# Optimization experiments

Hardware: AMD Instinct MI355X
Metric: run time of the kernel (lower is better)

Reference implementation:

```python
import jax, jax.numpy as jnp
import numpy as np

N = 100000   # nodes
E = 1600000  # edges
D = 128      # input_dim
H = 128      # hidden_dim
CH = 16      # cluster_hidden_dim
P = 10       # processor_nodes


def setup_inputs() -> dict:
    key = jax.random.key(0)
    ks = jax.random.split(key, 22)
    s = 0.05
    return {
        "x": jax.random.normal(ks[0], (N, D), jnp.float32),
        "edges": jax.random.randint(ks[1], (2, E), 0, N, dtype=jnp.int32),
        "edge_attr": jax.random.uniform(ks[2], (E,), jnp.float32),
        "ready": jax.random.randint(ks[3], (N, 1), 0, 2, dtype=jnp.int32),
        "proc_emb": jax.random.normal(ks[4], (P, 3), jnp.float32),
        # GCN layers (PyG GCNConv: lin without bias, explicit bias added after aggregation)
        "gcn_w": jax.random.normal(ks[5], (2, D, H), jnp.float32) * s,
        "gcn_b": jax.random.normal(ks[6], (2, H), jnp.float32) * s,
        # listmlp: Linear(H,H) -> relu, then Linear(H,1)
        "mlp_w1": jax.random.normal(ks[7], (H, H), jnp.float32) * s,
        "mlp_b1": jax.random.normal(ks[8], (H,), jnp.float32) * s,
        "mlp_w2": jax.random.normal(ks[9], (H, 1), jnp.float32) * s,
        "mlp_b2": jax.random.normal(ks[10], (1,), jnp.float32) * s,
        # listmlp_value: Linear(H,1)
        "val_w": jax.random.normal(ks[11], (H, 1), jnp.float32) * s,
        "val_b": jax.random.normal(ks[12], (1,), jnp.float32) * s,
        # cluster_linear: Linear(3*P, CH)
        "cl_w": jax.random.normal(ks[13], (3 * P, CH), jnp.float32) * s,
        "cl_b": jax.random.normal(ks[14], (CH,), jnp.float32) * s,
        # listmlp_pass: Linear(H+CH,H) -> relu, then Linear(H,1)
        "pass_w1": jax.random.normal(ks[15], (H + CH, H), jnp.float32) * s,
        "pass_b1": jax.random.normal(ks[16], (H,), jnp.float32) * s,
        "pass_w2": jax.random.normal(ks[17], (H, 1), jnp.float32) * s,
        "pass_b2": jax.random.normal(ks[18], (1,), jnp.float32) * s,
    }


def _gcn_layer(x, row, col, w_e, W, b):
    # PyG GCNConv with flow='target_to_source': out[row] += norm_e * (x @ W)[col]
    # gcn_norm with idx=row: deg[i] = sum of edge weights with row==i (self-loops included)
    h = x @ W                                              # [N,H]
    deg = jax.ops.segment_sum(w_e, row, num_segments=N)    # [N]
    dis = jnp.where(deg > 0, jax.lax.rsqrt(deg), 0.0)      # deg^-1/2, inf -> 0
    norm = dis[row] * w_e * dis[col]                       # [E+N]
    msg = h[col] * norm[:, None]                           # [E+N,H] gather
    out = jax.ops.segment_sum(msg, row, num_segments=N)    # [N,H] scatter-add
    return out + b


def _forward(x, edges, edge_attr, ready, proc_emb, gcn_w, gcn_b,
             mlp_w1, mlp_b1, mlp_w2, mlp_b2, val_w, val_b, cl_w, cl_b,
             pass_w1, pass_b1, pass_w2, pass_b2):
    # add self-loops with weight 1 (GCNConv default add_self_loops=True)
    loop = jnp.arange(N, dtype=edges.dtype)
    row = jnp.concatenate([edges[0], loop])
    col = jnp.concatenate([edges[1], loop])
    w_e = jnp.concatenate([edge_attr, jnp.ones((N,), edge_attr.dtype)])

    h = x
    for l in range(2):
        h = jax.nn.relu(_gcn_layer(h, row, col, w_e, gcn_w[l], gcn_b[l]))

    mask = ready[:, 0] > 0                                 # [N] bool
    v = jnp.mean(h, axis=0)                                # [H]
    x_pass = jnp.max(jnp.where(mask[:, None], h, -jnp.inf), axis=0)  # masked max, [H]

    fc = proc_emb.reshape(-1) @ cl_w + cl_b                # [CH]
    x_pass = jnp.concatenate([x_pass, fc], axis=0)         # [H+CH]

    v = v @ val_w + val_b                                  # [1]

    logits = jax.nn.relu(h @ mlp_w1 + mlp_b1) @ mlp_w2 + mlp_b2        # [N,1]
    x_pass = jax.nn.relu(x_pass @ pass_w1 + pass_b1) @ pass_w2 + pass_b2  # [1]

    # torch indexes logits[ready]; here we mask non-ready entries with -inf so
    # the softmax over [N+1] matches torch's values on the ready rows.
    node_logits = jnp.where(mask, logits[:, 0], -jnp.inf)
    probs = jax.nn.softmax(jnp.concatenate([node_logits, x_pass], axis=0))  # [N+1]
    return probs, v


def reference(x, edges, edge_attr, ready, proc_emb, gcn_w, gcn_b,
              mlp_w1, mlp_b1, mlp_w2, mlp_b2, val_w, val_b, cl_w, cl_b,
              pass_w1, pass_b1, pass_w2, pass_b2):
    return _forward(x, edges, edge_attr, ready, proc_emb, gcn_w, gcn_b,
                    mlp_w1, mlp_b1, mlp_w2, mlp_b2, val_w, val_b, cl_w, cl_b,
                    pass_w1, pass_b1, pass_w2, pass_b2)
```

## Files before the change

kernel.cpp:

```cpp
#include <hip/hip_runtime.h>
#include <cstdint>

#define NN 100000
#define EE 1600000
#define HH 128
#define NREP 8
#define PSZ (NN / 8)
#define HPP (PSZ / 2)
#define SS 64
#define CAP 300000
#define NBB 500
#define BCH 3200
#define SCAN_CHUNK 512
#define NSCAN ((NN + SCAN_CHUNK - 1) / SCAN_CHUNK)

typedef unsigned long long u64;
typedef unsigned short ushort;
typedef unsigned char uchar;
typedef __attribute__((ext_vector_type(8))) short bf16x8;
typedef __attribute__((ext_vector_type(4))) float f32x4;
typedef __attribute__((ext_vector_type(2))) float f32x2;

__device__ __forceinline__ void gl2lds16(const void* g, void* l) {
#if __has_builtin(__builtin_amdgcn_global_load_lds)
    __builtin_amdgcn_global_load_lds(
        (const __attribute__((address_space(1))) unsigned int*)g,
        (__attribute__((address_space(3))) unsigned int*)l, 16, 0, 0);
#else
    *(uint4*)l = *(const uint4*)g;
#endif
}

__device__ __forceinline__ ushort f2bf(float x) {
    union { float f; unsigned u; } v; v.f = x;
    unsigned r = v.u + 0x7fffu + ((v.u >> 16) & 1u);
    return (ushort)(r >> 16);
}
__device__ __forceinline__ float bf2f(unsigned h16) {
    union { unsigned u; float f; } v; v.u = h16 << 16; return v.f;
}

__device__ __forceinline__ uchar f2fp8(float a) {
    return (uchar)(__builtin_amdgcn_cvt_pk_fp8_f32(a, a, 0, false) & 0xff);
}
__device__ __forceinline__ void unpack8_fp8(uint2 q, float* v) {
    f32x2 a = __builtin_amdgcn_cvt_pk_f32_fp8(q.x, false);
    f32x2 b = __builtin_amdgcn_cvt_pk_f32_fp8(q.x, true);
    f32x2 c = __builtin_amdgcn_cvt_pk_f32_fp8(q.y, false);
    f32x2 d = __builtin_amdgcn_cvt_pk_f32_fp8(q.y, true);
    v[0] = a[0]; v[1] = a[1]; v[2] = b[0]; v[3] = b[1];
    v[4] = c[0]; v[5] = c[1]; v[6] = d[0]; v[7] = d[1];
}

__device__ __forceinline__ unsigned encf(float f) {
    int b = __float_as_int(f);
    return (b >= 0) ? ((unsigned)b | 0x80000000u) : ~(unsigned)b;
}
__device__ __forceinline__ float decf(unsigned u) {
    return (u & 0x80000000u) ? __int_as_float((int)(u & 0x7fffffffu))
                             : __int_as_float((int)(~u));
}
#define ENC_NEG_INF 0x007FFFFFu

__global__ void k_setup(float* __restrict__ meansum, unsigned* __restrict__ maxenc,
                        unsigned* __restrict__ lmaxenc, float* __restrict__ esum,
                        int* __restrict__ gtail,
                        const float* __restrict__ w0, const float* __restrict__ w1,
                        const float* __restrict__ w2, ushort* __restrict__ wt) {
    int idx = blockIdx.x * blockDim.x + threadIdx.x;
    if (idx < NREP * HH) { meansum[idx] = 0.f; maxenc[idx] = ENC_NEG_INF; }
    if (idx < 8) gtail[idx] = 0;
    if (idx == 0) { lmaxenc[0] = ENC_NEG_INF; esum[0] = 0.f; }
    if (idx < 3 * HH * HH) {
        int mat = idx >> 14;
        int e = idx & 16383;
        int n = e >> 7, k = e & 127;
        int g = k >> 3, el = k & 7;
        const float* src = (mat == 0) ? w0 : (mat == 1) ? w1 : w2;
        int pos = (mat << 14) | (n << 7) | (((g ^ (n & 15)) << 3) | el);
        wt[pos] = f2bf(src[k * HH + n]);
    }
}

__global__ __launch_bounds__(256) void k_bucket(const int* __restrict__ rows,
                                                const int* __restrict__ cols,
                                                const float* __restrict__ ea,
                                                int* __restrict__ gtail,
                                                u64* __restrict__ ebuck) {
    __shared__ u64 buf[8][1024];
    __shared__ int cnt8[8];
    __shared__ int rsv[8];
    int t = threadIdx.x;
    if (t < 8) cnt8[t] = 0;
    __syncthreads();
    int e0 = blockIdx.x * BCH;
    int e1 = e0 + BCH;
    for (int ebase = e0; ebase < e1; ebase += 1024) {
        int e = ebase + t * 4;
        if (e < e1) {
            int4 r4 = *(const int4*)(rows + e);
            int4 c4 = *(const int4*)(cols + e);
            float4 a4 = *(const float4*)(ea + e);
            int rr[4] = {r4.x, r4.y, r4.z, r4.w};
            int cc[4] = {c4.x, c4.y, c4.z, c4.w};
            float aa[4] = {a4.x, a4.y, a4.z, a4.w};
#pragma unroll
            for (int j = 0; j < 4; ++j) {
                int p = rr[j] / PSZ;
                int rl = rr[j] - p * PSZ;
                unsigned q = (unsigned)(aa[j] * 32767.0f + 0.5f);
                u64 en = ((u64)rl << 32) | (u64)(((unsigned)cc[j] << 15) | q);
                int idx = atomicAdd(&cnt8[p], 1);
                buf[p][idx] = en;
            }
        }
        __syncthreads();
        if (t < 8) rsv[t] = atomicAdd(&gtail[t], cnt8[t]);
        __syncthreads();
#pragma unroll
        for (int p = 0; p < 8; ++p) {
            int nn = cnt8[p], oo = rsv[p];
            u64* dst = ebuck + (size_t)p * CAP + oo;
            for (int j = t; j < nn; j += 256) dst[j] = buf[p][j];
        }
        __syncthreads();
        if (t < 8) cnt8[t] = 0;
        __syncthreads();
    }
}

__global__ __launch_bounds__(256) void k_cnt2(const u64* __restrict__ ebuck,
                                              const int* __restrict__ gtail,
                                              unsigned* __restrict__ cntp) {
    __shared__ unsigned h32[HPP];
    int b = blockIdx.x;
    int s = b >> 3, p = b & 7;
    for (int j = threadIdx.x; j < HPP; j += 256) h32[j] = 0;
    __syncthreads();
    int pc = gtail[p];
    int len = (pc + SS - 1) / SS;
    int lo = s * len, hi = min(lo + len, pc);
    const u64* src = ebuck + (size_t)p * CAP;
    for (int i = lo + threadIdx.x; i < hi; i += 256) {
        int rl = (int)(src[i] >> 32);
        atomicAdd(&h32[rl >> 1], (rl & 1) ? 0x10000u : 1u);
    }
    __syncthreads();
    unsigned* dst = cntp + (size_t)(p * SS + s) * HPP;
    for (int j = threadIdx.x; j < HPP; j += 256) dst[j] = h32[j];
}

__global__ void k_cntscan(const unsigned* __restrict__ cntp, int* __restrict__ count,
                          unsigned* __restrict__ deltap, int* __restrict__ basep,
                          int* __restrict__ bsum) {
    int b = blockIdx.x, t = threadIdx.x;
    int rp = b * 256 + t;
    int c0 = 0, c1 = 0;
    if (rp < NN / 2) {
        int p = rp / HPP, j = rp - p * HPP;
        unsigned s0 = 0, s1 = 0;
#pragma unroll 8
        for (int c = 0; c < SS; ++c) {
            size_t o = (size_t)(p * SS + c) * HPP + j;
            unsigned v = cntp[o];
            deltap[o] = s0 | (s1 << 16);
            s0 += v & 0xffffu;
            s1 += v >> 16;
        }
        c0 = (int)s0; c1 = (int)s1;
        *(int2*)(count + 2 * rp) = make_int2(c0, c1);
    }
    c0 = (c0 + 7) & ~7;
    c1 = (c1 + 7) & ~7;
    int s = c0 + c1;
    int lane = t & 63, w = t >> 6;
    int v = s;
#pragma unroll
    for (int off = 1; off < 64; off <<= 1) {
        int u = __shfl_up(v, off, 64);
        if (lane >= off) v += u;
    }
    __shared__ int wsum[4];
    if (lane == 63) wsum[w] = v;
    __syncthreads();
    int wadd = 0;
    for (int j = 0; j < w; ++j) wadd += wsum[j];
    int incl = v + wadd;
    int excl = incl - s;
    int i0 = 2 * rp;
    if (i0 < NN) basep[i0] = excl;
    if (i0 + 1 < NN) basep[i0 + 1] = excl + c0;
    if (t == 255) bsum[b] = incl;
}

__global__ void k_scan2(int* __restrict__ bsum, int* __restrict__ base) {
    __shared__ int tmp[256];
    int t = threadIdx.x;
    int v = (t < NSCAN) ? bsum[t] : 0;
    tmp[t] = v;
    __syncthreads();
    for (int off = 1; off < 256; off <<= 1) {
        int u = (t >= off) ? tmp[t - off] : 0;
        __syncthreads();
        tmp[t] += u;
        __syncthreads();
    }
    if (t == NSCAN - 1) base[NN] = tmp[t];
    if (t < NSCAN) bsum[t] = tmp[t] - v;
}

__global__ __launch_bounds__(256) void k_fill2(const u64* __restrict__ ebuck,
                                               const int* __restrict__ gtail,
                                               const unsigned* __restrict__ deltap,
                                               const int* __restrict__ basep,
                                               const int* __restrict__ bsum,
                                               unsigned* __restrict__ csre) {
    __shared__ int nxt[PSZ];
    int b = blockIdx.x;
    int s = b >> 3, p = b & 7;
    const unsigned* dsrc = deltap + (size_t)(p * SS + s) * HPP;
    const int* bsrc = basep + p * PSZ;
    for (int j = threadIdx.x; j < HPP; j += 256) {
        unsigned d = dsrc[j];
        int2 bb = *(const int2*)(bsrc + 2 * j);
        int badd = bsum[(p * PSZ + 2 * j) >> 9];
        nxt[2 * j] = bb.x + badd + (int)(d & 0xffffu);
        nxt[2 * j + 1] = bb.y + badd + (int)(d >> 16);
    }
    __syncthreads();
    int pc = gtail[p];
    int len = (pc + SS - 1) / SS;
    int lo = s * len, hi = min(lo + len, pc);
    const u64* src = ebuck + (size_t)p * CAP;
    for (int i = lo + threadIdx.x; i < hi; i += 256) {
        u64 en = src[i];
        int rl = (int)(en >> 32);
        int slot = atomicAdd(&nxt[rl], 1);
        csre[slot] = (unsigned)(en & 0xffffffffu);
    }
}

__global__ void k_degsum(const int* __restrict__ count, unsigned* __restrict__ csre,
                         const int* __restrict__ basep, const int* __restrict__ bsum,
                         int* __restrict__ base, float* __restrict__ dis) {
    int r = blockIdx.x * blockDim.x + threadIdx.x;
    if (r >= NN) return;
    int lo = basep[r] + bsum[r >> 9];
    int hip = (r == NN - 1) ? base[NN] : (basep[r + 1] + bsum[(r + 1) >> 9]);
    base[r] = lo;
    int hireal = lo + count[r];
    float s = 0.f;
    for (int e = lo; e < hireal; ++e) s += (float)(csre[e] & 0x7fffu);
    unsigned selfv = (unsigned)r << 15;
    for (int e = hireal; e < hip; ++e) csre[e] = selfv;
    dis[r] = rsqrtf(1.0f + s * (1.0f / 32767.0f));
}

__global__ __launch_bounds__(256) void k_gather(const uchar* __restrict__ hW,
                                                const unsigned* __restrict__ csre,
                                                const int* __restrict__ base,
                                                const float* __restrict__ dis,
                                                const float* __restrict__ bias,
                                                ushort* __restrict__ agg) {
    int node = blockIdx.x * 16 + (threadIdx.x >> 4);
    if (node >= NN) return;
    int l = threadIdx.x & 15;
    int f = l * 8;
    int lo = base[node], hi = base[node + 1];
    float disn = dis[node];
    float wk = disn * (1.0f / 32767.0f);
    float acc[8];
    {
        uint2 q = *(const uint2*)(hW + (size_t)node * HH + f);
        float v[8]; unpack8_fp8(q, v);
#pragma unroll
        for (int j = 0; j < 8; ++j) acc[j] = disn * v[j];
    }
    for (int eb = lo; eb < hi; eb += 8) {
        uint4 pa = *(const uint4*)(csre + eb);
        uint4 pb = *(const uint4*)(csre + eb + 4);
        unsigned pp[8] = {pa.x, pa.y, pa.z, pa.w, pb.x, pb.y, pb.z, pb.w};
        uint2 qq[8];
#pragma unroll
        for (int j = 0; j < 8; ++j)
            qq[j] = *(const uint2*)(hW + (size_t)(pp[j] >> 15) * HH + f);
#pragma unroll
        for (int j = 0; j < 8; ++j) {
            float w = (float)(pp[j] & 0x7fffu) * wk;
            float v[8]; unpack8_fp8(qq[j], v);
#pragma unroll
            for (int k = 0; k < 8; ++k) acc[k] += w * v[k];
        }
    }
    float4 b0 = *(const float4*)(bias + f);
    float4 b1 = *(const float4*)(bias + f + 4);
    ushort o[8];
    o[0] = f2bf(fmaxf(acc[0] + b0.x, 0.f)); o[1] = f2bf(fmaxf(acc[1] + b0.y, 0.f));
    o[2] = f2bf(fmaxf(acc[2] + b0.z, 0.f)); o[3] = f2bf(fmaxf(acc[3] + b0.w, 0.f));
    o[4] = f2bf(fmaxf(acc[4] + b1.x, 0.f)); o[5] = f2bf(fmaxf(acc[5] + b1.y, 0.f));
    o[6] = f2bf(fmaxf(acc[6] + b1.z, 0.f)); o[7] = f2bf(fmaxf(acc[7] + b1.w, 0.f));
    int gsw = (l ^ (node & 15)) * 8;
    *(uint4*)(agg + (size_t)node * HH + gsw) = *(uint4*)o;
}

template <int MODE>
__global__ __launch_bounds__(256) void k_mfma(const void* __restrict__ Ain,
                                              const ushort* __restrict__ Wt,
                                              uchar* __restrict__ C,
                                              const float* __restrict__ dis,
                                              const float* __restrict__ b1,
                                              const float* __restrict__ w2v,
                                              const float* __restrict__ b2,
                                              const int* __restrict__ ready,
                                              float* __restrict__ logits,
                                              float* __restrict__ meansum,
                                              unsigned* __restrict__ maxenc,
                                              unsigned* __restrict__ lmaxenc, int n) {
    __shared__ ushort As[64 * HH];
    __shared__ ushort Ws[128 * HH];
    __shared__ int rdy[64];
    __shared__ unsigned slmax;
    const int t = threadIdx.x;
    const int rb = blockIdx.x * 64;
    const int wv = t >> 6, ln = t & 63;

    {
        const char* wsb = (const char*)Wt;
        char* wdb = (char*)Ws;
#pragma unroll
        for (int i = 0; i < 8; ++i) {
            int blk = wv * 8 + i;
            gl2lds16(wsb + blk * 1024 + ln * 16, wdb + blk * 1024);
        }
    }
    if (MODE != 0) {
        const char* asb = (const char*)Ain + (size_t)rb * HH * 2;
        char* adb = (char*)As;
#pragma unroll
        for (int i = 0; i < 4; ++i) {
            int blk = wv * 4 + i;
            gl2lds16(asb + blk * 1024 + ln * 16, adb + blk * 1024);
        }
    } else {
#pragma unroll
        for (int i = 0; i < 4; ++i) {
            int m = i * 16 + (t >> 4);
            int k = (t & 15) * 8;
            ushort pk[8];
            const float* Af = (const float*)Ain;
            float4 v0 = make_float4(0.f, 0.f, 0.f, 0.f), v1 = v0;
            if (rb + m < n) {
                const float* src = Af + (size_t)(rb + m) * HH + k;
                v0 = *(const float4*)src;
                v1 = *(const float4*)(src + 4);
            }
            pk[0] = f2bf(v0.x); pk[1] = f2bf(v0.y); pk[2] = f2bf(v0.z); pk[3] = f2bf(v0.w);
            pk[4] = f2bf(v1.x); pk[5] = f2bf(v1.y); pk[6] = f2bf(v1.z); pk[7] = f2bf(v1.w);
            int gsw = (t & 15) ^ (m & 15);
            *(uint4*)(As + m * HH + gsw * 8) = *(uint4*)pk;
        }
    }
    if (MODE == 2) {
        if (t < 64) rdy[t] = (rb + t < n) ? ready[rb + t] : 0;
        if (t == 0) slmax = ENC_NEG_INF;
    }
    __syncthreads();

    const int cl = ln & 15;
    const int kq = ln >> 4;
    const int m0 = wv * 16;

    f32x4 acc[8];
#pragma unroll
    for (int c = 0; c < 8; ++c) acc[c] = (f32x4){0.f, 0.f, 0.f, 0.f};

#pragma unroll
    for (int kk = 0; kk < 4; ++kk) {
        int g = kk * 4 + kq;
        bf16x8 bfr = *(const bf16x8*)(As + (m0 + cl) * HH + ((g ^ cl) * 8));
#pragma unroll
        for (int c = 0; c < 8; ++c) {
            bf16x8 afr = *(const bf16x8*)(Ws + (c * 16 + cl) * HH + ((g ^ cl) * 8));
            acc[c] = __builtin_amdgcn_mfma_f32_16x16x32_bf16(afr, bfr, acc[c], 0, 0, 0);
        }
    }

    const int node = rb + m0 + cl;
    if (MODE < 2) {
        if (node < n) {
            float d = dis[node];
            uchar* dst = C + (size_t)node * HH + kq * 4;
#pragma unroll
            for (int c = 0; c < 8; ++c) {
                unsigned u = __builtin_amdgcn_cvt_pk_fp8_f32(acc[c][0] * d, acc[c][1] * d, 0u, false);
                u = __builtin_amdgcn_cvt_pk_fp8_f32(acc[c][2] * d, acc[c][3] * d, u, true);
                *(unsigned*)(dst + c * 16) = u;
            }
        }
    } else {
        float s = 0.f;
#pragma unroll
        for (int c = 0; c < 8; ++c) {
            float4 bb = *(const float4*)(b1 + c * 16 + kq * 4);
            float4 ww = *(const float4*)(w2v + c * 16 + kq * 4);
            s += fmaxf(acc[c][0] + bb.x, 0.f) * ww.x;
            s += fmaxf(acc[c][1] + bb.y, 0.f) * ww.y;
            s += fmaxf(acc[c][2] + bb.z, 0.f) * ww.z;
            s += fmaxf(acc[c][3] + bb.w, 0.f) * ww.w;
        }
        s += __shfl_xor(s, 16, 64);
        s += __shfl_xor(s, 32, 64);
        unsigned mylmax = ENC_NEG_INF;
        if (kq == 0 && node < n) {
            float lg = s + b2[0];
            logits[node] = lg;
            if (rdy[m0 + cl] > 0) mylmax = encf(lg);
        }
        if (mylmax != ENC_NEG_INF) atomicMax(&slmax, mylmax);

        int lim = min(64, n - rb);
        if (t < HH) {
            int f = t, gf = f >> 3, fo = f & 7;
            float sum = 0.f, mx = -3.4e38f;
            for (int m = 0; m < lim; ++m) {
                float v = bf2f(As[m * HH + ((gf ^ (m & 15)) * 8) + fo]);
                sum += v;
                if (rdy[m] > 0) mx = fmaxf(mx, v);
            }
            int rep = blockIdx.x & (NREP - 1);
            atomicAdd(&meansum[rep * HH + f], sum);
            if (mx > -3.0e38f) atomicMax(&maxenc[rep * HH + f], encf(mx));
        }
        __syncthreads();
        if (t == 0 && slmax != ENC_NEG_INF) atomicMax(lmaxenc, slmax);
    }
}

__global__ void k_fin1(const float* __restrict__ meansum, const unsigned* __restrict__ maxenc,
                       const unsigned* __restrict__ lmaxenc,
                       const float* __restrict__ val_w, const float* __restrict__ val_b,
                       const float* __restrict__ pe, const float* __restrict__ cl_w,
                       const float* __restrict__ cl_b, const float* __restrict__ pw1,
                       const float* __restrict__ pb1, const float* __restrict__ pw2,
                       const float* __restrict__ pb2, float* __restrict__ scal,
                       float* __restrict__ d_out) {
    __shared__ float xp[144];
    __shared__ float msum[HH];
    __shared__ float zp[HH];
    int t = threadIdx.x;
    if (t < HH) {
        float s = 0.f;
        unsigned mx = ENC_NEG_INF;
#pragma unroll
        for (int r = 0; r < NREP; ++r) {
            s += meansum[r * HH + t];
            unsigned e = maxenc[r * HH + t];
            if (e > mx) mx = e;
        }
        msum[t] = s;
        xp[t] = decf(mx);
    } else if (t < 144) {
        int c = t - HH;
        float s = cl_b[c];
        for (int k = 0; k < 30; ++k) s += pe[k] * cl_w[k * 16 + c];
        xp[t] = s;
    }
    __syncthreads();
    if (t < HH) {
        float s = pb1[t];
        for (int k = 0; k < 144; ++k) s += xp[k] * pw1[k * HH + t];
        zp[t] = fmaxf(s, 0.f);
    }
    __syncthreads();
    if (t < 64) {
        float s1 = zp[t] * pw2[t] + zp[t + 64] * pw2[t + 64];
        float s2 = msum[t] * val_w[t] + msum[t + 64] * val_w[t + 64];
#pragma unroll
        for (int off = 32; off > 0; off >>= 1) {
            s1 += __shfl_xor(s1, off, 64);
            s2 += __shfl_xor(s2, off, 64);
        }
        if (t == 0) {
            float xpass = s1 + pb2[0];
            float v = s2 * (1.0f / NN) + val_b[0];
            float M = fmaxf(decf(lmaxenc[0]), xpass);
            scal[0] = M;
            scal[1] = expf(xpass - M);
            d_out[NN + 1] = v;
        }
    }
}

__global__ __launch_bounds__(256) void k_exp(const float* __restrict__ logits,
                                             const int* __restrict__ ready,
                                             const float* __restrict__ scal,
                                             float* __restrict__ d_out,
                                             float* __restrict__ esum) {
    __shared__ float warr[4];
    int t = threadIdx.x;
    int i = blockIdx.x * 256 + t;
    float M = scal[0];
    float p = 0.f;
    if (i < NN) {
        if (ready[i] > 0) p = expf(logits[i] - M);
        d_out[i] = p;
    }
    float s = p;
#pragma unroll
    for (int off = 32; off > 0; off >>= 1) s += __shfl_xor(s, off, 64);
    if ((t & 63) == 0) warr[t >> 6] = s;
    __syncthreads();
    if (t == 0) atomicAdd(esum, warr[0] + warr[1] + warr[2] + warr[3]);
}

__global__ void k_scale(const float* __restrict__ esum, const float* __restrict__ scal,
                        float* __restrict__ d_out) {
    int i = blockIdx.x * blockDim.x + threadIdx.x;
    float inv = 1.0f / (esum[0] + scal[1]);
    if (i < NN) d_out[i] *= inv;
    else if (i == NN) d_out[NN] = scal[1] * inv;
}

extern "C" void kernel_launch(void* const* d_in, const int* in_sizes, int n_in,
                              void* d_out, int out_size, void* d_ws, size_t ws_size,
                              hipStream_t stream) {
    const float* x      = (const float*)d_in[0];
    const int*   edges  = (const int*)d_in[1];
    const float* eattr  = (const float*)d_in[2];
    const int*   ready  = (const int*)d_in[3];
    const float* pe     = (const float*)d_in[4];
    const float* gcn_w  = (const float*)d_in[5];
    const float* gcn_b  = (const float*)d_in[6];
    const float* mlp_w1 = (const float*)d_in[7];
    const float* mlp_b1 = (const float*)d_in[8];
    const float* mlp_w2 = (const float*)d_in[9];
    const float* mlp_b2 = (const float*)d_in[10];
    const float* val_w  = (const float*)d_in[11];
    const float* val_b  = (const float*)d_in[12];
    const float* cl_w   = (const float*)d_in[13];
    const float* cl_b   = (const float*)d_in[14];
    const float* pw1    = (const float*)d_in[15];
    const float* pb1    = (const float*)d_in[16];
    const float* pw2    = (const float*)d_in[17];
    const float* pb2    = (const float*)d_in[18];

    const int* rows = edges;
    const int* cols = edges + EE;

    char* P = (char*)d_ws;
    size_t off = 0;
    auto carve = [&](size_t bytes) {
        off = (off + 255) & ~(size_t)255;
        void* p = P + off;
        off += bytes;
        return p;
    };
    float* dis     = (float*)carve(NN * 4);
    float* logits  = (float*)carve(NN * 4);
    int*   count   = (int*)carve(NN * 4);
    int*   basep   = (int*)carve(NN * 4);
    int*   base    = (int*)carve((NN + 1) * 4);
    int*   bsum    = (int*)carve(256 * 4);
    ushort* bufB   = (ushort*)carve((size_t)NN * HH * 2);
    uchar* bufH    = (uchar*)carve((size_t)NN * HH);
    unsigned* csre = (unsigned*)carve((size_t)(EE + 8 * NN) * 4);
    u64*   ebuck   = (u64*)carve((size_t)8 * CAP * 8);
    float* meansum = (float*)carve(NREP * HH * 4);
    unsigned* maxenc = (unsigned*)carve(NREP * HH * 4);
    unsigned* lmaxenc = (unsigned*)carve(4);
    float* esum    = (float*)carve(4);
    float* scal    = (float*)carve(8);
    int*   gtail   = (int*)carve(8 * 4);
    ushort* wt     = (ushort*)carve(3 * HH * HH * 2);

    unsigned* cntp   = (unsigned*)bufB;
    unsigned* deltap = (unsigned*)bufB + (size_t)8 * SS * HPP;

    float* out = (float*)d_out;

    const int nb = (NN + 255) / 256;
    const int gb = (NN + 63) / 64;
    const int ab = (NN + 15) / 16;
    const int pb = 8 * SS;

    k_setup<<<(3 * HH * HH + 255) / 256, 256, 0, stream>>>(meansum, maxenc, lmaxenc, esum,
                                                           gtail, gcn_w, gcn_w + HH * HH,
                                                           mlp_w1, wt);

    k_bucket<<<NBB, 256, 0, stream>>>(rows, cols, eattr, gtail, ebuck);
    k_cnt2<<<pb, 256, 0, stream>>>(ebuck, gtail, cntp);
    k_cntscan<<<NSCAN, 256, 0, stream>>>(cntp, count, deltap, basep, bsum);
    k_scan2<<<1, 256, 0, stream>>>(bsum, base);
    k_fill2<<<pb, 256, 0, stream>>>(ebuck, gtail, deltap, basep, bsum, csre);
    k_degsum<<<nb, 256, 0, stream>>>(count, csre, basep, bsum, base, dis);

    k_mfma<0><<<gb, 256, 0, stream>>>(x, wt, bufH, dis, nullptr, nullptr, nullptr, nullptr,
                                      nullptr, nullptr, nullptr, nullptr, NN);
    k_gather<<<ab, 256, 0, stream>>>(bufH, csre, base, dis, gcn_b, bufB);

    k_mfma<1><<<gb, 256, 0, stream>>>(bufB, wt + HH * HH, bufH, dis, nullptr, nullptr, nullptr,
                                      nullptr, nullptr, nullptr, nullptr, nullptr, NN);
    k_gather<<<ab, 256, 0, stream>>>(bufH, csre, base, dis, gcn_b + HH, bufB);

    k_mfma<2><<<gb, 256, 0, stream>>>(bufB, wt + 2 * HH * HH, nullptr, nullptr, mlp_b1, mlp_w2,
                                      mlp_b2, ready, logits, meansum, maxenc, lmaxenc, NN);
    k_fin1<<<1, 256, 0, stream>>>(meansum, maxenc, lmaxenc, val_w, val_b, pe, cl_w, cl_b,
                                  pw1, pb1, pw2, pb2, scal, out);
    k_exp<<<nb, 256, 0, stream>>>(logits, ready, scal, out, esum);
    k_scale<<<(NN + 1 + 255) / 256, 256, 0, stream>>>(esum, scal, out);
}
```

Baseline: 335.2 us.

## Stage fp8 output through LDS, split column reduce, widen atomic replicas

In MODE<2, the fp8 GEMM output is now staged in shared memory with a padded row stride and then written as contiguous 32-byte chunks per thread, replacing scattered 4-byte stores. In MODE 2, the per-feature mean/max reduction over 64 rows is split across all 256 threads (two halves combined through shared memory) instead of using only 128 threads. The number of atomic replica slots grows from 8 to 64 to reduce contention. The costs are two extra barriers, and the finalize kernel must sum over more replicas.

Result: no change. 330.6 us (-1.4%).

```diff
diff --git a/kernel.cpp b/kernel.cpp
--- a/kernel.cpp
+++ b/kernel.cpp
@@ -4,7 +4,7 @@
 #define NN 100000
 #define EE 1600000
 #define HH 128
-#define NREP 8
+#define NREP 64
 #define PSZ (NN / 8)
 #define HPP (PSZ / 2)
 #define SS 64
@@ -316,9 +316,11 @@
                                               float* __restrict__ meansum,
                                               unsigned* __restrict__ maxenc,
                                               unsigned* __restrict__ lmaxenc, int n) {
-    __shared__ ushort As[64 * HH];
+    __shared__ __align__(16) ushort As[64 * HH];
     __shared__ ushort Ws[128 * HH];
     __shared__ int rdy[64];
+    __shared__ float xs[128];
+    __shared__ float xmf[128];
     __shared__ unsigned slmax;
     const int t = threadIdx.x;
     const int rb = blockIdx.x * 64;
@@ -387,15 +389,23 @@
 
     const int node = rb + m0 + cl;
     if (MODE < 2) {
-        if (node < n) {
-            float d = dis[node];
-            uchar* dst = C + (size_t)node * HH + kq * 4;
-#pragma unroll
-            for (int c = 0; c < 8; ++c) {
-                unsigned u = __builtin_amdgcn_cvt_pk_fp8_f32(acc[c][0] * d, acc[c][1] * d, 0u, false);
-                u = __builtin_amdgcn_cvt_pk_fp8_f32(acc[c][2] * d, acc[c][3] * d, u, true);
-                *(unsigned*)(dst + c * 16) = u;
-            }
+        float d = (node < n) ? dis[node] : 0.f;
+        uchar* Cs = (uchar*)As;
+        __syncthreads();
+#pragma unroll
+        for (int c = 0; c < 8; ++c) {
+            unsigned u = __builtin_amdgcn_cvt_pk_fp8_f32(acc[c][0] * d, acc[c][1] * d, 0u, false);
+            u = __builtin_amdgcn_cvt_pk_fp8_f32(acc[c][2] * d, acc[c][3] * d, u, true);
+            *(unsigned*)(Cs + (m0 + cl) * 144 + c * 16 + kq * 4) = u;
+        }
+        __syncthreads();
+        int row = t >> 2, off = (t & 3) * 32;
+        if (rb + row < n) {
+            uint4 q0 = *(const uint4*)(Cs + row * 144 + off);
+            uint4 q1 = *(const uint4*)(Cs + row * 144 + off + 16);
+            uchar* dst = C + (size_t)(rb + row) * HH + off;
+            *(uint4*)dst = q0;
+            *(uint4*)(dst + 16) = q1;
         }
     } else {
         float s = 0.f;
@@ -419,17 +429,25 @@
         if (mylmax != ENC_NEG_INF) atomicMax(&slmax, mylmax);
 
         int lim = min(64, n - rb);
-        if (t < HH) {
-            int f = t, gf = f >> 3, fo = f & 7;
+        {
+            int f = t & 127, h = t >> 7;
+            int gf = f >> 3, fo = f & 7;
             float sum = 0.f, mx = -3.4e38f;
-            for (int m = 0; m < lim; ++m) {
+            int mlo = h * 32, mhi = min(lim, mlo + 32);
+            for (int m = mlo; m < mhi; ++m) {
                 float v = bf2f(As[m * HH + ((gf ^ (m & 15)) * 8) + fo]);
                 sum += v;
                 if (rdy[m] > 0) mx = fmaxf(mx, v);
             }
-            int rep = blockIdx.x & (NREP - 1);
-            atomicAdd(&meansum[rep * HH + f], sum);
-            if (mx > -3.0e38f) atomicMax(&maxenc[rep * HH + f], encf(mx));
+            if (h == 0) { xs[f] = sum; xmf[f] = mx; }
+            __syncthreads();
+            if (h == 1) {
+                sum += xs[f];
+                mx = fmaxf(mx, xmf[f]);
+                int rep = blockIdx.x & (NREP - 1);
+                atomicAdd(&meansum[rep * HH + f], sum);
+                if (mx > -3.0e38f) atomicMax(&maxenc[rep * HH + f], encf(mx));
+            }
         }
         __syncthreads();
         if (t == 0 && slmax != ENC_NEG_INF) atomicMax(lmaxenc, slmax);
@@ -451,7 +469,6 @@
     if (t < HH) {
         float s = 0.f;
         unsigned mx = ENC_NEG_INF;
-#pragma unroll
         for (int r = 0; r < NREP; ++r) {
             s += meansum[r * HH + t];
             unsigned e = maxenc[r * HH + t];
```
